# Kernel optimization log

Hardware: AMD Instinct MI355X
Metric: run time of the kernel (lower is better)

The kernel has to match this reference:

```python
import jax, jax.numpy as jnp
import numpy as np

GAMMA = 2.0  # args.gamma
B, C, H, W = 8, 21, 512, 512


def setup_inputs() -> dict:
    key = jax.random.key(0)
    k1, k2 = jax.random.split(key)
    pred = jax.random.normal(k1, (B, C, H, W), dtype=jnp.float32)
    # one-hot target built from random per-pixel class labels
    labels = jax.random.randint(k2, (B, H, W), 0, C)
    target = jax.nn.one_hot(labels, C, dtype=jnp.float32)  # [B,H,W,C]
    target = jnp.transpose(target, (0, 3, 1, 2))  # [B,C,H,W]
    return {"pred": pred, "target": target}


def reference(pred, target) -> jnp.ndarray:
    b, c, h, w = pred.shape
    logits = jax.nn.log_softmax(pred, axis=1)  # [B,C,H,W]
    lo = jnp.transpose(logits, (0, 2, 3, 1)).reshape(-1, c)  # [N,C]
    tg = jnp.transpose(target, (0, 2, 3, 1)).reshape(-1, c)  # [N,C]
    n = lo.shape[0]
    beta = (n - 1.0) / n
    # per-pixel focal term summed over channels: sum_j (1-p_j)^gamma * log p_j * t_j
    row_val = jnp.sum((1.0 - jnp.exp(lo)) ** GAMMA * lo * tg, axis=1)  # [N]
    mask = (tg == 1).astype(lo.dtype)  # [N,C] class membership mask
    n_c = jnp.sum(mask, axis=0)  # [C] pixels per class
    class_sum = jnp.einsum('nc,n->c', mask, row_val)  # [C] masked reductions
    w = (1.0 - beta) / (1.0 - jnp.power(jnp.float32(beta), n_c) + 1e-6)  # [C]
    return -jnp.sum(w * class_sum) / n
```

## Files before the change

kernel.cpp:

```cpp
#include <hip/hip_runtime.h>

#define CCH    21
#define HWSZ   (512*512)
#define HW4    (HWSZ/4)
#define NPIX   (8*HWSZ)
#define BLKT   256
#define NBLK   (NPIX/4/BLKT)
#define PF     4

#define WAIT_VM(n) __builtin_amdgcn_s_waitcnt(0x0F70 | (n))

typedef float vfloat4 __attribute__((ext_vector_type(4)));

__global__ __launch_bounds__(BLKT) void cb_focal_partial(
    const float* __restrict__ pred, const float* __restrict__ targ,
    float* __restrict__ gsum, float* __restrict__ gcnt)
{
    __shared__ float ls_sum[CCH];
    __shared__ float ls_cnt[CCH];
    if (threadIdx.x < CCH) { ls_sum[threadIdx.x] = 0.f; ls_cnt[threadIdx.x] = 0.f; }
    __syncthreads();

    const int tid = blockIdx.x * BLKT + threadIdx.x;
    const int b   = tid >> 16;
    const int hw4 = tid & (HW4 - 1);
    const float* pp = pred + (size_t)b * CCH * HWSZ + (size_t)hw4 * 4;
    const float* tp = targ + (size_t)b * CCH * HWSZ + (size_t)hw4 * 4;

    float s0 = 0.f, s1 = 0.f, s2 = 0.f, s3 = 0.f;
    float vy0 = 0.f, vy1 = 0.f, vy2 = 0.f, vy3 = 0.f;
    float ey0 = 1.f, ey1 = 1.f, ey2 = 1.f, ey3 = 1.f;
    int   y0 = 0, y1 = 0, y2 = 0, y3 = 0;

    vfloat4 pv[PF], tv[PF];

    #pragma unroll
    for (int c = 0; c < PF; ++c) {
        pv[c] = *(const vfloat4*)(pp + (size_t)c * HWSZ);
        tv[c] = *(const vfloat4*)(tp + (size_t)c * HWSZ);
        __builtin_amdgcn_sched_barrier(0);
    }

    #pragma unroll
    for (int c = 0; c < CCH; ++c) {
        if      (c <= CCH - 4) { WAIT_VM(6); }
        else if (c == CCH - 3) { WAIT_VM(4); }
        else if (c == CCH - 2) { WAIT_VM(2); }
        else                   { WAIT_VM(0); }
        __builtin_amdgcn_sched_barrier(0);

        const vfloat4 p = pv[c % PF];
        const vfloat4 t = tv[c % PF];

        if (c + PF < CCH) {
            pv[c % PF] = *(const vfloat4*)(pp + (size_t)(c + PF) * HWSZ);
            tv[c % PF] = *(const vfloat4*)(tp + (size_t)(c + PF) * HWSZ);
        }
        __builtin_amdgcn_sched_barrier(0);

        const float e0 = __expf(p.x), e1 = __expf(p.y),
                    e2 = __expf(p.z), e3 = __expf(p.w);
        s0 += e0; s1 += e1; s2 += e2; s3 += e3;
        const bool h0 = t.x > 0.5f, h1 = t.y > 0.5f,
                   h2 = t.z > 0.5f, h3 = t.w > 0.5f;
        y0 = h0 ? c : y0;  vy0 = h0 ? p.x : vy0;  ey0 = h0 ? e0 : ey0;
        y1 = h1 ? c : y1;  vy1 = h1 ? p.y : vy1;  ey1 = h1 ? e1 : ey1;
        y2 = h2 ? c : y2;  vy2 = h2 ? p.z : vy2;  ey2 = h2 ? e2 : ey2;
        y3 = h3 ? c : y3;  vy3 = h3 ? p.w : vy3;  ey3 = h3 ? e3 : ey3;
    }

    {
        const float l0 = vy0 - __logf(s0), p0 = ey0 / s0, o0 = 1.f - p0;
        const float l1 = vy1 - __logf(s1), p1 = ey1 / s1, o1 = 1.f - p1;
        const float l2 = vy2 - __logf(s2), p2 = ey2 / s2, o2 = 1.f - p2;
        const float l3 = vy3 - __logf(s3), p3 = ey3 / s3, o3 = 1.f - p3;
        atomicAdd(&ls_sum[y0], o0 * o0 * l0);  atomicAdd(&ls_cnt[y0], 1.f);
        atomicAdd(&ls_sum[y1], o1 * o1 * l1);  atomicAdd(&ls_cnt[y1], 1.f);
        atomicAdd(&ls_sum[y2], o2 * o2 * l2);  atomicAdd(&ls_cnt[y2], 1.f);
        atomicAdd(&ls_sum[y3], o3 * o3 * l3);  atomicAdd(&ls_cnt[y3], 1.f);
    }
    __syncthreads();
    if (threadIdx.x < CCH) {
        atomicAdd(&gsum[threadIdx.x], ls_sum[threadIdx.x]);
        atomicAdd(&gcnt[threadIdx.x], ls_cnt[threadIdx.x]);
    }
}

__global__ void cb_focal_final(const float* __restrict__ gsum,
                               const float* __restrict__ gcnt,
                               float* __restrict__ out)
{
    const int lane = threadIdx.x;
    double term = 0.0;
    if (lane < CCH) {
        const double n    = (double)NPIX;
        const double beta = (n - 1.0) / n;
        const double w = (1.0 - beta) / (1.0 - pow(beta, (double)gcnt[lane]) + 1e-6);
        term = w * (double)gsum[lane];
    }
    for (int off = 32; off; off >>= 1) term += __shfl_down(term, off, 64);
    if (lane == 0) out[0] = (float)(-term / (double)NPIX);
}

extern "C" void kernel_launch(void* const* d_in, const int* in_sizes, int n_in,
                              void* d_out, int out_size, void* d_ws, size_t ws_size,
                              hipStream_t stream) {
    const float* pred = (const float*)d_in[0];
    const float* targ = (const float*)d_in[1];
    float* out  = (float*)d_out;
    float* gsum = (float*)d_ws;
    float* gcnt = gsum + CCH;

    (void)hipMemsetAsync(gsum, 0, 2 * CCH * sizeof(float), stream);
    cb_focal_partial<<<NBLK, BLKT, 0, stream>>>(pred, targ, gsum, gcnt);
    cb_focal_final<<<1, 64, 0, stream>>>(gsum, gcnt, out);
}
```

Measured before the change: 360.3 us.

## Stage target loads through LDS via global_load_lds with 3-channel stage pipeline

Routes target tensor loads directly into shared memory with global_load_lds and loads pred with nontemporal loads. Channels are processed in groups of three with one group prefetched ahead. Each stage waits for all outstanding loads (vmcnt 0) before consuming the next group. This frees VGPRs and bypasses cache pollution, but replaces the finer rolling wait of the old four-deep prefetch with a coarser full drain per stage. It also adds an LDS dependency per stage.

```diff
diff --git a/kernel.cpp b/kernel.cpp
--- a/kernel.cpp
+++ b/kernel.cpp
@@ -6,16 +6,25 @@
 #define NPIX   (8*HWSZ)
 #define BLKT   256
 #define NBLK   (NPIX/4/BLKT)
-#define PF     4
+#define CS     3
+#define NS     7
 
-#define WAIT_VM(n) __builtin_amdgcn_s_waitcnt(0x0F70 | (n))
+#define WAIT_VM0   __builtin_amdgcn_s_waitcnt(0x0F70)
+#define WAIT_LGKM0 __builtin_amdgcn_s_waitcnt(0xC07F)
 
 typedef float vfloat4 __attribute__((ext_vector_type(4)));
+
+__device__ __forceinline__ void stage16(const float* g, vfloat4* l) {
+    __builtin_amdgcn_global_load_lds(
+        (const __attribute__((address_space(1))) unsigned int*)g,
+        (__attribute__((address_space(3))) unsigned int*)l, 16, 0, 0);
+}
 
 __global__ __launch_bounds__(BLKT) void cb_focal_partial(
     const float* __restrict__ pred, const float* __restrict__ targ,
     float* __restrict__ gsum, float* __restrict__ gcnt)
 {
+    __shared__ vfloat4 tbuf[CS][BLKT];
     __shared__ float ls_sum[CCH];
     __shared__ float ls_cnt[CCH];
     if (threadIdx.x < CCH) { ls_sum[threadIdx.x] = 0.f; ls_cnt[threadIdx.x] = 0.f; }
@@ -26,47 +35,62 @@
     const int hw4 = tid & (HW4 - 1);
     const float* pp = pred + (size_t)b * CCH * HWSZ + (size_t)hw4 * 4;
     const float* tp = targ + (size_t)b * CCH * HWSZ + (size_t)hw4 * 4;
+    const int wv = threadIdx.x & 192;
 
     float s0 = 0.f, s1 = 0.f, s2 = 0.f, s3 = 0.f;
     float vy0 = 0.f, vy1 = 0.f, vy2 = 0.f, vy3 = 0.f;
     float ey0 = 1.f, ey1 = 1.f, ey2 = 1.f, ey3 = 1.f;
     int   y0 = 0, y1 = 0, y2 = 0, y3 = 0;
 
-    vfloat4 pv[PF], tv[PF];
+    vfloat4 pn[CS];
 
     #pragma unroll
-    for (int c = 0; c < PF; ++c) {
-        pv[c] = *(const vfloat4*)(pp + (size_t)c * HWSZ);
-        tv[c] = *(const vfloat4*)(tp + (size_t)c * HWSZ);
-        __builtin_amdgcn_sched_barrier(0);
-    }
+    for (int j = 0; j < CS; ++j)
+        stage16(tp + (size_t)j * HWSZ, &tbuf[j][wv]);
+    #pragma unroll
+    for (int j = 0; j < CS; ++j)
+        pn[j] = __builtin_nontemporal_load((const vfloat4*)(pp + (size_t)j * HWSZ));
+    __builtin_amdgcn_sched_barrier(0);
 
     #pragma unroll
-    for (int c = 0; c < CCH; ++c) {
-        if      (c <= CCH - 4) { WAIT_VM(6); }
-        else if (c == CCH - 3) { WAIT_VM(4); }
-        else if (c == CCH - 2) { WAIT_VM(2); }
-        else                   { WAIT_VM(0); }
+    for (int s = 0; s < NS; ++s) {
+        WAIT_VM0;
         __builtin_amdgcn_sched_barrier(0);
 
-        const vfloat4 p = pv[c % PF];
-        const vfloat4 t = tv[c % PF];
+        vfloat4 pv[CS], tv[CS];
+        #pragma unroll
+        for (int j = 0; j < CS; ++j) pv[j] = pn[j];
+        #pragma unroll
+        for (int j = 0; j < CS; ++j) tv[j] = tbuf[j][threadIdx.x];
+        WAIT_LGKM0;
+        __builtin_amdgcn_sched_barrier(0);
 
-        if (c + PF < CCH) {
-            pv[c % PF] = *(const vfloat4*)(pp + (size_t)(c + PF) * HWSZ);
-            tv[c % PF] = *(const vfloat4*)(tp + (size_t)(c + PF) * HWSZ);
+        if (s + 1 < NS) {
+            #pragma unroll
+            for (int j = 0; j < CS; ++j)
+                stage16(tp + (size_t)((s + 1) * CS + j) * HWSZ, &tbuf[j][wv]);
+            #pragma unroll
+            for (int j = 0; j < CS; ++j)
+                pn[j] = __builtin_nontemporal_load(
+                    (const vfloat4*)(pp + (size_t)((s + 1) * CS + j) * HWSZ));
         }
         __builtin_amdgcn_sched_barrier(0);
 
-        const float e0 = __expf(p.x), e1 = __expf(p.y),
-                    e2 = __expf(p.z), e3 = __expf(p.w);
-        s0 += e0; s1 += e1; s2 += e2; s3 += e3;
-        const bool h0 = t.x > 0.5f, h1 = t.y > 0.5f,
-                   h2 = t.z > 0.5f, h3 = t.w > 0.5f;
-        y0 = h0 ? c : y0;  vy0 = h0 ? p.x : vy0;  ey0 = h0 ? e0 : ey0;
-        y1 = h1 ? c : y1;  vy1 = h1 ? p.y : vy1;  ey1 = h1 ? e1 : ey1;
-        y2 = h2 ? c : y2;  vy2 = h2 ? p.z : vy2;  ey2 = h2 ? e2 : ey2;
-        y3 = h3 ? c : y3;  vy3 = h3 ? p.w : vy3;  ey3 = h3 ? e3 : ey3;
+        #pragma unroll
+        for (int j = 0; j < CS; ++j) {
+            const int c = s * CS + j;
+            const vfloat4 p = pv[j];
+            const vfloat4 t = tv[j];
+            const float e0 = __expf(p.x), e1 = __expf(p.y),
+                        e2 = __expf(p.z), e3 = __expf(p.w);
+            s0 += e0; s1 += e1; s2 += e2; s3 += e3;
+            const bool h0 = t.x > 0.5f, h1 = t.y > 0.5f,
+                       h2 = t.z > 0.5f, h3 = t.w > 0.5f;
+            y0 = h0 ? c : y0;  vy0 = h0 ? p.x : vy0;  ey0 = h0 ? e0 : ey0;
+            y1 = h1 ? c : y1;  vy1 = h1 ? p.y : vy1;  ey1 = h1 ? e1 : ey1;
+            y2 = h2 ? c : y2;  vy2 = h2 ? p.z : vy2;  ey2 = h2 ? e2 : ey2;
+            y3 = h3 ? c : y3;  vy3 = h3 ? p.w : vy3;  ey3 = h3 ? e3 : ey3;
+        }
     }
 
     {
```

Measured after the change: 355.6 us. No clear change (-1.3%).
